# Kernel tuning notes

Measured on AMD Instinct MI355X. Metric: run time of the kernel, lower is better.

## Reference

```python
import jax, jax.numpy as jnp
import numpy as np

FLOAT_MAX = 3.4e38
FLOAT_MIN = -3.4e38


def _net1_forward(link_mtx, action_mask, col_table, rel_table, graph_weight,
                  graph_bias, Wk, Wq, Wv, fc_w, table_ids, l_col_ids, r_col_ids):
    emb = rel_table.shape[1]

    # ---- graph_forward: GCN layer over relation graph, mean pooling ----
    # link_mtx: [B, R, R], rel_table: [R, E]
    support = jnp.einsum('bnm,me->bne', link_mtx, rel_table)          # [B, R, E]
    out_graph = jax.nn.relu(support @ graph_weight + graph_bias)      # [B, R, G]
    pooled = out_graph.mean(axis=1)                                   # [B, G]

    # ---- tree_forward: batched left-deep join trees via scan over depth ----
    # table_ids: [B, T, D+1]; col ids: [B, T, D, C]
    r_tabs = rel_table[table_ids[..., 1:]]                            # [B, T, D, E]
    l_cols = col_table[l_col_ids].mean(axis=-2)                       # [B, T, D, E] (mean pooling of joined cols)
    r_cols = col_table[r_col_ids].mean(axis=-2)                       # [B, T, D, E]
    xs = (jnp.moveaxis(r_tabs, 2, 0), jnp.moveaxis(l_cols, 2, 0),
          jnp.moveaxis(r_cols, 2, 0))                                  # each [D, B, T, E]
    init = rel_table[table_ids[..., 0]]                               # [B, T, E] leftmost leaf

    def step(prev, x):
        rte, lce, rce = x
        # query_emb = cat([l_table, l_col, r_col, r_table]) -> 4 tokens
        q = jnp.stack([prev, lce, rce, rte], axis=-2)                 # [B, T, 4, E]
        K = q @ Wk
        Q = q @ Wq
        V = q @ Wv
        scores = jnp.einsum('btqe,btke->btqk', Q, K) / emb            # note: /emb, not /sqrt(emb)
        attn = jax.nn.softmax(scores, axis=-1)
        out = jnp.einsum('btqk,btke->btqe', attn, V).sum(axis=-2)     # sum over query rows -> [B, T, E]
        return out, None

    final, _ = jax.lax.scan(step, init, xs)                           # [B, T, E]
    tree_emb = final.sum(axis=1)                                      # sum over subtrees -> [B, E]

    logits = jnp.concatenate([pooled, tree_emb], axis=1) @ fc_w       # [B, A]
    inf_mask = jnp.clip(jnp.log(action_mask), FLOAT_MIN, FLOAT_MAX)
    return inf_mask + logits


def setup_inputs() -> dict:
    key = jax.random.key(0)
    ks = jax.random.split(key, 12)
    B, T, D, C = 8, 8, 16, 2
    num_rel, num_col, num_actions = 4096, 20000, 4096
    emb, gdim = 64, 64
    std = 0.05
    return {
        'link_mtx': jax.random.uniform(ks[0], (B, num_rel, num_rel), dtype=jnp.float32),
        'action_mask': jnp.ones((B, num_actions), dtype=jnp.float32),
        'col_table': jax.random.normal(ks[1], (num_col, emb), dtype=jnp.float32) * std,
        'rel_table': jax.random.normal(ks[2], (num_rel, emb), dtype=jnp.float32) * std,
        'graph_weight': jax.random.normal(ks[3], (emb, gdim), dtype=jnp.float32) * std,
        'graph_bias': jnp.zeros((gdim,), dtype=jnp.float32),
        'Wk': jax.random.normal(ks[4], (emb, emb), dtype=jnp.float32) * std,
        'Wq': jax.random.normal(ks[5], (emb, emb), dtype=jnp.float32) * std,
        'Wv': jax.random.normal(ks[6], (emb, emb), dtype=jnp.float32) * std,
        'fc_w': jax.random.normal(ks[7], (gdim + emb, num_actions), dtype=jnp.float32) * std,
        'table_ids': jax.random.randint(ks[8], (B, T, D + 1), 0, num_rel),
        'l_col_ids': jax.random.randint(ks[9], (B, T, D, C), 0, num_col),
        'r_col_ids': jax.random.randint(ks[10], (B, T, D, C), 0, num_col),
    }


def reference(link_mtx, action_mask, col_table, rel_table, graph_weight,
              graph_bias, Wk, Wq, Wv, fc_w, table_ids, l_col_ids, r_col_ids):
    return _net1_forward(link_mtx, action_mask, col_table, rel_table, graph_weight,
                         graph_bias, Wk, Wq, Wv, fc_w, table_ids, l_col_ids, r_col_ids)
```

## Files before the change

### kernel.cpp

```cpp
#include <hip/hip_runtime.h>
#include <hip/hip_bf16.h>
#include <stdint.h>

typedef __attribute__((ext_vector_type(8))) short short8;
typedef __attribute__((ext_vector_type(4))) float f32x4;

union FragU { short8 s; __hip_bfloat162 h[4]; };
union BU { uint4 u; short8 s; };

__device__ __forceinline__ unsigned short f2bf(float f) {
  union { float f; unsigned int u; } v; v.f = f;
  unsigned int r = v.u + 0x7fffu + ((v.u >> 16) & 1u);
  return (unsigned short)(r >> 16);
}
__device__ __forceinline__ float bf2f(unsigned short h) {
  union { unsigned int u; float f; } v; v.u = ((unsigned int)h) << 16;
  return v.f;
}

#define GLOAD_LDS16(gp, lp) \
  __builtin_amdgcn_global_load_lds((const __attribute__((address_space(1))) void*)(gp), \
                                   (__attribute__((address_space(3))) void*)(lp), 16, 0, 0)

__global__ void k_prep(const float* __restrict__ rel, const float* __restrict__ GW,
                       unsigned short* __restrict__ bTf, float* __restrict__ accums) {
  __shared__ float tile[64][65];
  __shared__ float gws[64][64];
  __shared__ float relgw[64][64];
  const int j = blockIdx.x;
  const int t = threadIdx.x;
#pragma unroll
  for (int p = 0; p < 16; ++p) {
    int elem = p * 256 + t;
    int kk = elem >> 6, ee = elem & 63;
    tile[kk][ee] = rel[(j * 64 + kk) * 64 + ee];
    ((float*)gws)[elem] = GW[elem];
  }
  __syncthreads();
  {
    const int e = t >> 2, chunk = t & 3;
    for (int i = 0; i < 16; ++i) {
      float acc = 0.f;
#pragma unroll
      for (int ii = 0; ii < 64; ++ii) acc += tile[chunk * 16 + i][ii] * gws[ii][e];
      relgw[chunk * 16 + i][e] = acc;
    }
  }
  __syncthreads();
#pragma unroll
  for (int m = 0; m < 2; ++m) {
    const int f = t * 2 + m;
    const int nt = f >> 7, kc = (f >> 6) & 1, ln = f & 63;
    const int g = ln >> 4, r = ln & 15;
    union { unsigned short u16[8]; uint4 v; } pk;
#pragma unroll
    for (int s = 0; s < 8; ++s) pk.u16[s] = f2bf(relgw[kc * 32 + g * 8 + s][nt * 16 + r]);
    *(uint4*)(bTf + (size_t)j * 4096 + f * 8) = pk.v;
  }
  if (j == 0) {
    accums[t] = 0.f; accums[t + 256] = 0.f; accums[t + 512] = 0.f; accums[t + 768] = 0.f;
  }
}

__global__ __launch_bounds__(256, 2) void k_main(
    const float* __restrict__ link, const unsigned short* __restrict__ bTf,
    const float* __restrict__ gbias, float* __restrict__ pooled_sum,
    const float* __restrict__ col_table, const float* __restrict__ rel_table,
    const float* __restrict__ Wk, const float* __restrict__ Wq, const float* __restrict__ Wv,
    const int* __restrict__ table_ids, const int* __restrict__ l_ids,
    const int* __restrict__ r_ids, float* __restrict__ tree_emb) {
  __shared__ union {
    struct { char a[4][2][8192]; } g;
    struct { unsigned short W3b[3 * 4096]; float qT[4][64][4]; } tr;
  } sm;

  const int t = threadIdx.x;
  const int lane = t & 63;
  const int wid = t >> 6;

  if (blockIdx.x >= 16) {
    const int gid = blockIdx.x - 16;
    const int b = gid >> 6;
    const int rb = gid & 63;
    const int rowG0 = rb * 64 + wid * 16;
    const int phase = (gid * 4 + wid + b * 9) & 31;
    const int g = lane >> 4;
    const int r = lane & 15;
    const uint32_t fr = (uint32_t)((r & 7) << 4);

    const char* linkb = (const char*)(link + ((size_t)b << 24));
    const char* bTfb = (const char*)bTf;
    const int a_r2 = lane >> 5;
    const uint32_t a_wb = (uint32_t)((lane & 31) * 16);

    char* a0buf = sm.g.a[wid][0];
    char* a1buf = sm.g.a[wid][1];

    f32x4 acc[4];
#pragma unroll
    for (int nt = 0; nt < 4; ++nt) acc[nt] = (f32x4){0.f, 0.f, 0.f, 0.f};
    uint4 bq[16];

#define STAGEA(ab_, tta) do {                                              \
    const size_t ka = (size_t)(tta) * 512;          \
    _Pragma("unroll")                                                      \
    for (int j = 0; j < 8; ++j) {                                          \
      const int wlrow = 2 * j + a_r2;                                      \
      const uint32_t cb = a_wb ^ ((uint32_t)(wlrow & 7) << 4);             \
      GLOAD_LDS16(linkb + (size_t)(rowG0 + wlrow) * 16384 + ka + cb,       \
                  (ab_) + j * 1024);                                       \
    }                                                                      \
  } while (0)

#define LOADB(tta) do {                                                    \
    const char* bb = bTfb + (size_t)(tta) * 16384 + lane * 16;             \
    _Pragma("unroll")                                                      \
    for (int j = 0; j < 8; ++j) {                                          \
      bq[j]     = *(const uint4*)(bb + j * 1024);                          \
      bq[8 + j] = *(const uint4*)(bb + 8192 + j * 1024);                   \
    }                                                                      \
  } while (0)

#define COMPUTEW(ab_) do {                                                 \
    const char* ar = (ab_) + r * 512;                                      \
    _Pragma("unroll")                                                      \
    for (int kh = 0; kh < 2; ++kh) {                                       \
      _Pragma("unroll")                                                    \
      for (int kc = 0; kc < 2; ++kc) {                                     \
        const uint32_t o0 = ((uint32_t)(kh * 256 + kc * 128 + g * 32)) ^ fr; \
        const f32x4 a0 = *(const f32x4*)(ar + o0);                         \
        const f32x4 a1 = *(const f32x4*)(ar + (o0 ^ 16));                  \
        FragU f;                                                           \
        f.h[0] = __float22bfloat162_rn(float2{a0[0], a0[1]});              \
        f.h[1] = __float22bfloat162_rn(float2{a0[2], a0[3]});              \
        f.h[2] = __float22bfloat162_rn(float2{a1[0], a1[1]});              \
        f.h[3] = __float22bfloat162_rn(float2{a1[2], a1[3]});              \
        _Pragma("unroll")                                                  \
        for (int nt = 0; nt < 4; ++nt) {                                   \
          BU bu; bu.u = bq[kh * 8 + nt * 2 + kc];                          \
          acc[nt] = __builtin_amdgcn_mfma_f32_16x16x32_bf16(f.s, bu.s, acc[nt], 0, 0, 0); \
        }                                                                  \
      }                                                                    \
    }                                                                      \
  } while (0)

    STAGEA(a0buf, phase);
    for (int it2 = 0; it2 < 16; ++it2) {
      const int te = 2 * it2;
      LOADB((te + phase) & 31);
      STAGEA(a1buf, (te + 1 + phase) & 31);
      asm volatile("s_waitcnt vmcnt(8)" ::: "memory");
      COMPUTEW(a0buf);
      LOADB((te + 1 + phase) & 31);
      if (it2 < 15) {
        STAGEA(a0buf, (te + 2 + phase) & 31);
        asm volatile("s_waitcnt vmcnt(8)" ::: "memory");
      } else {
        asm volatile("s_waitcnt vmcnt(0)" ::: "memory");
      }
      COMPUTEW(a1buf);
    }

#pragma unroll
    for (int nt = 0; nt < 4; ++nt) {
      const float gbv = gbias[nt * 16 + r];
      float s = 0.f;
#pragma unroll
      for (int j = 0; j < 4; ++j) s += fmaxf(acc[nt][j] + gbv, 0.f);
      s += __shfl_xor(s, 16);
      s += __shfl_xor(s, 32);
      if (g == 0) atomicAdd(&pooled_sum[b * 64 + nt * 16 + r], s);
    }
  } else {
    const int e = lane;
    for (int i = t; i < 3 * 4096; i += 256) {
      float v;
      if (i < 4096) v = Wk[i];
      else if (i < 8192) v = Wq[i - 4096];
      else v = Wv[i - 8192];
      sm.tr.W3b[i] = f2bf(v);
    }
    __syncthreads();

    const int tree = blockIdx.x * 4 + wid;
    const int b = tree >> 3;
    const int* tid = table_ids + tree * 17;
    const int* lid = l_ids + tree * 32;
    const int* rid = r_ids + tree * 32;

    float prev = rel_table[tid[0] * 64 + e];

    for (int d = 0; d < 16; ++d) {
      const int l0 = lid[d * 2], l1 = lid[d * 2 + 1];
      const int r0 = rid[d * 2], r1 = rid[d * 2 + 1];
      const float lce = 0.5f * (col_table[l0 * 64 + e] + col_table[l1 * 64 + e]);
      const float rce = 0.5f * (col_table[r0 * 64 + e] + col_table[r1 * 64 + e]);
      const float rte = rel_table[tid[1 + d] * 64 + e];
      float4 qv0; qv0.x = prev; qv0.y = lce; qv0.z = rce; qv0.w = rte;
      *(float4*)&sm.tr.qT[wid][e][0] = qv0;
      __syncthreads();

      float K[4] = {0, 0, 0, 0}, Q[4] = {0, 0, 0, 0}, V[4] = {0, 0, 0, 0};
#pragma unroll 8
      for (int i = 0; i < 64; ++i) {
        const f32x4 qv = *(const f32x4*)&sm.tr.qT[wid][i][0];
        const float wk = bf2f(sm.tr.W3b[i * 64 + e]);
        const float wq = bf2f(sm.tr.W3b[4096 + i * 64 + e]);
        const float wvv = bf2f(sm.tr.W3b[8192 + i * 64 + e]);
#pragma unroll
        for (int j = 0; j < 4; ++j) {
          K[j] += qv[j] * wk;
          Q[j] += qv[j] * wq;
          V[j] += qv[j] * wvv;
        }
      }

      float sc[4][4];
#pragma unroll
      for (int j = 0; j < 4; ++j)
#pragma unroll
        for (int k = 0; k < 4; ++k) {
          float p = Q[j] * K[k];
          p += __shfl_xor(p, 1);  p += __shfl_xor(p, 2);  p += __shfl_xor(p, 4);
          p += __shfl_xor(p, 8);  p += __shfl_xor(p, 16); p += __shfl_xor(p, 32);
          sc[j][k] = p * (1.f / 64.f);
        }

      float wsum[4] = {0, 0, 0, 0};
#pragma unroll
      for (int j = 0; j < 4; ++j) {
        float mx = fmaxf(fmaxf(sc[j][0], sc[j][1]), fmaxf(sc[j][2], sc[j][3]));
        float a0 = __expf(sc[j][0] - mx), a1 = __expf(sc[j][1] - mx);
        float a2 = __expf(sc[j][2] - mx), a3 = __expf(sc[j][3] - mx);
        float inv = 1.f / (a0 + a1 + a2 + a3);
        wsum[0] += a0 * inv; wsum[1] += a1 * inv; wsum[2] += a2 * inv; wsum[3] += a3 * inv;
      }

      prev = wsum[0] * V[0] + wsum[1] * V[1] + wsum[2] * V[2] + wsum[3] * V[3];
      __syncthreads();
    }
    atomicAdd(&tree_emb[b * 64 + e], prev);
  }
}

__global__ void k_final(const float* __restrict__ action_mask, const float* __restrict__ fc_w,
                        const float* __restrict__ pooled_sum, const float* __restrict__ tree_emb,
                        float* __restrict__ out) {
  __shared__ float c[128];
  const int b = blockIdx.x >> 4;
  const int a = ((blockIdx.x & 15) << 8) + threadIdx.x;
  if (threadIdx.x < 128) {
    c[threadIdx.x] = (threadIdx.x < 64) ? pooled_sum[b * 64 + threadIdx.x] * (1.f / 4096.f)
                                        : tree_emb[b * 64 + threadIdx.x - 64];
  }
  __syncthreads();
  float acc = 0.f;
  for (int i = 0; i < 128; ++i) acc += c[i] * fc_w[i * 4096 + a];
  const float m = action_mask[b * 4096 + a];
  float lg = __logf(m);
  lg = fminf(fmaxf(lg, -3.4e38f), 3.4e38f);
  out[b * 4096 + a] = lg + acc;
}

extern "C" void kernel_launch(void* const* d_in, const int* in_sizes, int n_in,
                              void* d_out, int out_size, void* d_ws, size_t ws_size,
                              hipStream_t stream) {
  const float* link = (const float*)d_in[0];
  const float* mask = (const float*)d_in[1];
  const float* col = (const float*)d_in[2];
  const float* rel = (const float*)d_in[3];
  const float* GW = (const float*)d_in[4];
  const float* gb = (const float*)d_in[5];
  const float* Wk = (const float*)d_in[6];
  const float* Wq = (const float*)d_in[7];
  const float* Wv = (const float*)d_in[8];
  const float* fcw = (const float*)d_in[9];
  const int* tids = (const int*)d_in[10];
  const int* lids = (const int*)d_in[11];
  const int* rids = (const int*)d_in[12];
  float* out = (float*)d_out;

  unsigned short* bTf = (unsigned short*)d_ws;
  float* accums = (float*)((char*)d_ws + 512 * 1024);
  float* pooled_sum = accums;
  float* tree = accums + 512;

  hipLaunchKernelGGL(k_prep, dim3(64), dim3(256), 0, stream, rel, GW, bTf, accums);
  hipLaunchKernelGGL(k_main, dim3(528), dim3(256), 0, stream,
                     link, bTf, gb, pooled_sum,
                     col, rel, Wk, Wq, Wv, tids, lids, rids, tree);
  hipLaunchKernelGGL(k_final, dim3(128), dim3(256), 0, stream, mask, fcw, pooled_sum, tree, out);
}
```

Measured before the change: 142.9 us.

## Move tree attention blocks into prep kernel and zero accumulators via memset

The 16 tree-scan blocks move out of the main GEMM kernel and into the prep kernel, which now runs 80 blocks: 64 for the rel·GW precompute and 16 for the tree recurrence. Accumulator zeroing becomes a hipMemsetAsync instead of being done by block 0 of prep. The aim is to keep the slow serial tree blocks off the main kernel's critical path and to shrink its shared-memory union to the A staging buffers only. The cost is an extra memset launch, and the tree work now serialises with prep before the main kernel starts.

```diff
diff --git a/kernel.cpp b/kernel.cpp
--- a/kernel.cpp
+++ b/kernel.cpp
@@ -23,83 +23,152 @@
                                    (__attribute__((address_space(3))) void*)(lp), 16, 0, 0)
 
 __global__ void k_prep(const float* __restrict__ rel, const float* __restrict__ GW,
-                       unsigned short* __restrict__ bTf, float* __restrict__ accums) {
-  __shared__ float tile[64][65];
-  __shared__ float gws[64][64];
-  __shared__ float relgw[64][64];
-  const int j = blockIdx.x;
-  const int t = threadIdx.x;
-#pragma unroll
-  for (int p = 0; p < 16; ++p) {
-    int elem = p * 256 + t;
-    int kk = elem >> 6, ee = elem & 63;
-    tile[kk][ee] = rel[(j * 64 + kk) * 64 + ee];
-    ((float*)gws)[elem] = GW[elem];
-  }
-  __syncthreads();
-  {
-    const int e = t >> 2, chunk = t & 3;
-    for (int i = 0; i < 16; ++i) {
-      float acc = 0.f;
-#pragma unroll
-      for (int ii = 0; ii < 64; ++ii) acc += tile[chunk * 16 + i][ii] * gws[ii][e];
-      relgw[chunk * 16 + i][e] = acc;
-    }
-  }
-  __syncthreads();
-#pragma unroll
-  for (int m = 0; m < 2; ++m) {
-    const int f = t * 2 + m;
-    const int nt = f >> 7, kc = (f >> 6) & 1, ln = f & 63;
-    const int g = ln >> 4, r = ln & 15;
-    union { unsigned short u16[8]; uint4 v; } pk;
-#pragma unroll
-    for (int s = 0; s < 8; ++s) pk.u16[s] = f2bf(relgw[kc * 32 + g * 8 + s][nt * 16 + r]);
-    *(uint4*)(bTf + (size_t)j * 4096 + f * 8) = pk.v;
-  }
-  if (j == 0) {
-    accums[t] = 0.f; accums[t + 256] = 0.f; accums[t + 512] = 0.f; accums[t + 768] = 0.f;
-  }
-}
-
-__global__ __launch_bounds__(256, 2) void k_main(
-    const float* __restrict__ link, const unsigned short* __restrict__ bTf,
-    const float* __restrict__ gbias, float* __restrict__ pooled_sum,
-    const float* __restrict__ col_table, const float* __restrict__ rel_table,
-    const float* __restrict__ Wk, const float* __restrict__ Wq, const float* __restrict__ Wv,
-    const int* __restrict__ table_ids, const int* __restrict__ l_ids,
-    const int* __restrict__ r_ids, float* __restrict__ tree_emb) {
+                       unsigned short* __restrict__ bTf,
+                       const float* __restrict__ col_table, const float* __restrict__ rel_table,
+                       const float* __restrict__ Wk, const float* __restrict__ Wq,
+                       const float* __restrict__ Wv,
+                       const int* __restrict__ table_ids, const int* __restrict__ l_ids,
+                       const int* __restrict__ r_ids, float* __restrict__ tree_emb) {
   __shared__ union {
-    struct { char a[4][2][8192]; } g;
+    struct { float tile[64][65]; float gws[64][64]; float relgw[64][64]; } p;
     struct { unsigned short W3b[3 * 4096]; float qT[4][64][4]; } tr;
   } sm;
-
   const int t = threadIdx.x;
   const int lane = t & 63;
   const int wid = t >> 6;
 
-  if (blockIdx.x >= 16) {
-    const int gid = blockIdx.x - 16;
-    const int b = gid >> 6;
-    const int rb = gid & 63;
-    const int rowG0 = rb * 64 + wid * 16;
-    const int phase = (gid * 4 + wid + b * 9) & 31;
-    const int g = lane >> 4;
-    const int r = lane & 15;
-    const uint32_t fr = (uint32_t)((r & 7) << 4);
-
-    const char* linkb = (const char*)(link + ((size_t)b << 24));
-    const char* bTfb = (const char*)bTf;
-    const int a_r2 = lane >> 5;
-    const uint32_t a_wb = (uint32_t)((lane & 31) * 16);
-
-    char* a0buf = sm.g.a[wid][0];
-    char* a1buf = sm.g.a[wid][1];
-
-    f32x4 acc[4];
-#pragma unroll
-    for (int nt = 0; nt < 4; ++nt) acc[nt] = (f32x4){0.f, 0.f, 0.f, 0.f};
-    uint4 bq[16];
+  if (blockIdx.x < 64) {
+    const int j = blockIdx.x;
+#pragma unroll
+    for (int p = 0; p < 16; ++p) {
+      int elem = p * 256 + t;
+      int kk = elem >> 6, ee = elem & 63;
+      sm.p.tile[kk][ee] = rel[(j * 64 + kk) * 64 + ee];
+      ((float*)sm.p.gws)[elem] = GW[elem];
+    }
+    __syncthreads();
+    {
+      const int e = t >> 2, chunk = t & 3;
+      for (int i = 0; i < 16; ++i) {
+        float acc = 0.f;
+#pragma unroll
+        for (int ii = 0; ii < 64; ++ii) acc += sm.p.tile[chunk * 16 + i][ii] * sm.p.gws[ii][e];
+        sm.p.relgw[chunk * 16 + i][e] = acc;
+      }
+    }
+    __syncthreads();
+#pragma unroll
+    for (int m = 0; m < 2; ++m) {
+      const int f = t * 2 + m;
+      const int nt = f >> 7, kc = (f >> 6) & 1, ln = f & 63;
+      const int g = ln >> 4, r = ln & 15;
+      union { unsigned short u16[8]; uint4 v; } pk;
+#pragma unroll
+      for (int s = 0; s < 8; ++s) pk.u16[s] = f2bf(sm.p.relgw[kc * 32 + g * 8 + s][nt * 16 + r]);
+      *(uint4*)(bTf + (size_t)j * 4096 + f * 8) = pk.v;
+    }
+  } else {
+    const int e = lane;
+    for (int i = t; i < 3 * 4096; i += 256) {
+      float v;
+      if (i < 4096) v = Wk[i];
+      else if (i < 8192) v = Wq[i - 4096];
+      else v = Wv[i - 8192];
+      sm.tr.W3b[i] = f2bf(v);
+    }
+    __syncthreads();
+
+    const int tree = (blockIdx.x - 64) * 4 + wid;
+    const int b = tree >> 3;
+    const int* tid = table_ids + tree * 17;
+    const int* lid = l_ids + tree * 32;
+    const int* rid = r_ids + tree * 32;
+
+    float prev = rel_table[tid[0] * 64 + e];
+
+    for (int d = 0; d < 16; ++d) {
+      const int l0 = lid[d * 2], l1 = lid[d * 2 + 1];
+      const int r0 = rid[d * 2], r1 = rid[d * 2 + 1];
+      const float lce = 0.5f * (col_table[l0 * 64 + e] + col_table[l1 * 64 + e]);
+      const float rce = 0.5f * (col_table[r0 * 64 + e] + col_table[r1 * 64 + e]);
+      const float rte = rel_table[tid[1 + d] * 64 + e];
+      float4 qv0; qv0.x = prev; qv0.y = lce; qv0.z = rce; qv0.w = rte;
+      *(float4*)&sm.tr.qT[wid][e][0] = qv0;
+      __syncthreads();
+
+      float K[4] = {0, 0, 0, 0}, Q[4] = {0, 0, 0, 0}, V[4] = {0, 0, 0, 0};
+#pragma unroll 8
+      for (int i = 0; i < 64; ++i) {
+        const f32x4 qv = *(const f32x4*)&sm.tr.qT[wid][i][0];
+        const float wk = bf2f(sm.tr.W3b[i * 64 + e]);
+        const float wq = bf2f(sm.tr.W3b[4096 + i * 64 + e]);
+        const float wvv = bf2f(sm.tr.W3b[8192 + i * 64 + e]);
+#pragma unroll
+        for (int j = 0; j < 4; ++j) {
+          K[j] += qv[j] * wk;
+          Q[j] += qv[j] * wq;
+          V[j] += qv[j] * wvv;
+        }
+      }
+
+      float sc[4][4];
+#pragma unroll
+      for (int j = 0; j < 4; ++j)
+#pragma unroll
+        for (int k = 0; k < 4; ++k) {
+          float p = Q[j] * K[k];
+          p += __shfl_xor(p, 1);  p += __shfl_xor(p, 2);  p += __shfl_xor(p, 4);
+          p += __shfl_xor(p, 8);  p += __shfl_xor(p, 16); p += __shfl_xor(p, 32);
+          sc[j][k] = p * (1.f / 64.f);
+        }
+
+      float wsum[4] = {0, 0, 0, 0};
+#pragma unroll
+      for (int j = 0; j < 4; ++j) {
+        float mx = fmaxf(fmaxf(sc[j][0], sc[j][1]), fmaxf(sc[j][2], sc[j][3]));
+        float a0 = __expf(sc[j][0] - mx), a1 = __expf(sc[j][1] - mx);
+        float a2 = __expf(sc[j][2] - mx), a3 = __expf(sc[j][3] - mx);
+        float inv = 1.f / (a0 + a1 + a2 + a3);
+        wsum[0] += a0 * inv; wsum[1] += a1 * inv; wsum[2] += a2 * inv; wsum[3] += a3 * inv;
+      }
+
+      prev = wsum[0] * V[0] + wsum[1] * V[1] + wsum[2] * V[2] + wsum[3] * V[3];
+      __syncthreads();
+    }
+    atomicAdd(&tree_emb[b * 64 + e], prev);
+  }
+}
+
+__global__ __launch_bounds__(256, 2) void k_main(
+    const float* __restrict__ link, const unsigned short* __restrict__ bTf,
+    const float* __restrict__ gbias, float* __restrict__ pooled_sum) {
+  __shared__ char aLds[4][2][8192];
+
+  const int t = threadIdx.x;
+  const int lane = t & 63;
+  const int wid = t >> 6;
+
+  const int gid = blockIdx.x;
+  const int b = gid >> 6;
+  const int rb = gid & 63;
+  const int rowG0 = rb * 64 + wid * 16;
+  const int phase = (gid * 4 + wid + b * 9) & 31;
+  const int g = lane >> 4;
+  const int r = lane & 15;
+  const uint32_t fr = (uint32_t)((r & 7) << 4);
+
+  const char* linkb = (const char*)(link + ((size_t)b << 24));
+  const char* bTfb = (const char*)bTf;
+  const int a_r2 = lane >> 5;
+  const uint32_t a_wb = (uint32_t)((lane & 31) * 16);
+
+  char* a0buf = aLds[wid][0];
+  char* a1buf = aLds[wid][1];
+
+  f32x4 acc[4];
+#pragma unroll
+  for (int nt = 0; nt < 4; ++nt) acc[nt] = (f32x4){0.f, 0.f, 0.f, 0.f};
+  uint4 bq[16];
 
 #define STAGEA(ab_, tta) do {                                              \
     const size_t ka = (size_t)(tta) * 512;          \
@@ -144,102 +213,32 @@
     }                                                                      \
   } while (0)
 
-    STAGEA(a0buf, phase);
-    for (int it2 = 0; it2 < 16; ++it2) {
-      const int te = 2 * it2;
-      LOADB((te + phase) & 31);
-      STAGEA(a1buf, (te + 1 + phase) & 31);
+  STAGEA(a0buf, phase);
+  for (int it2 = 0; it2 < 16; ++it2) {
+    const int te = 2 * it2;
+    LOADB((te + phase) & 31);
+    STAGEA(a1buf, (te + 1 + phase) & 31);
+    asm volatile("s_waitcnt vmcnt(8)" ::: "memory");
+    COMPUTEW(a0buf);
+    LOADB((te + 1 + phase) & 31);
+    if (it2 < 15) {
+      STAGEA(a0buf, (te + 2 + phase) & 31);
       asm volatile("s_waitcnt vmcnt(8)" ::: "memory");
-      COMPUTEW(a0buf);
-      LOADB((te + 1 + phase) & 31);
-      if (it2 < 15) {
-        STAGEA(a0buf, (te + 2 + phase) & 31);
-        asm volatile("s_waitcnt vmcnt(8)" ::: "memory");
-      } else {
-        asm volatile("s_waitcnt vmcnt(0)" ::: "memory");
-      }
-      COMPUTEW(a1buf);
-    }
-
-#pragma unroll
-    for (int nt = 0; nt < 4; ++nt) {
-      const float gbv = gbias[nt * 16 + r];
-      float s = 0.f;
-#pragma unroll
-      for (int j = 0; j < 4; ++j) s += fmaxf(acc[nt][j] + gbv, 0.f);
-      s += __shfl_xor(s, 16);
-      s += __shfl_xor(s, 32);
-      if (g == 0) atomicAdd(&pooled_sum[b * 64 + nt * 16 + r], s);
-    }
-  } else {
-    const int e = lane;
-    for (int i = t; i < 3 * 4096; i += 256) {
-      float v;
-      if (i < 4096) v = Wk[i];
-      else if (i < 8192) v = Wq[i - 4096];
-      else v = Wv[i - 8192];
-      sm.tr.W3b[i] = f2bf(v);
-    }
-    __syncthreads();
-
-    const int tree = blockIdx.x * 4 + wid;
-    const int b = tree >> 3;
-    const int* tid = table_ids + tree * 17;
-    const int* lid = l_ids + tree * 32;
-    const int* rid = r_ids + tree * 32;
-
-    float prev = rel_table[tid[0] * 64 + e];
-
-    for (int d = 0; d < 16; ++d) {
-      const int l0 = lid[d * 2], l1 = lid[d * 2 + 1];
-      const int r0 = rid[d * 2], r1 = rid[d * 2 + 1];
-      const float lce = 0.5f * (col_table[l0 * 64 + e] + col_table[l1 * 64 + e]);
-      const float rce = 0.5f * (col_table[r0 * 64 + e] + col_table[r1 * 64 + e]);
-      const float rte = rel_table[tid[1 + d] * 64 + e];
-      float4 qv0; qv0.x = prev; qv0.y = lce; qv0.z = rce; qv0.w = rte;
-      *(float4*)&sm.tr.qT[wid][e][0] = qv0;
-      __syncthreads();
-
-      float K[4] = {0, 0, 0, 0}, Q[4] = {0, 0, 0, 0}, V[4] = {0, 0, 0, 0};
-#pragma unroll 8
-      for (int i = 0; i < 64; ++i) {
-        const f32x4 qv = *(const f32x4*)&sm.tr.qT[wid][i][0];
-        const float wk = bf2f(sm.tr.W3b[i * 64 + e]);
-        const float wq = bf2f(sm.tr.W3b[4096 + i * 64 + e]);
-        const float wvv = bf2f(sm.tr.W3b[8192 + i * 64 + e]);
-#pragma unroll
-        for (int j = 0; j < 4; ++j) {
-          K[j] += qv[j] * wk;
-          Q[j] += qv[j] * wq;
-          V[j] += qv[j] * wvv;
-        }
-      }
-
-      float sc[4][4];
-#pragma unroll
-      for (int j = 0; j < 4; ++j)
-#pragma unroll
-        for (int k = 0; k < 4; ++k) {
-          float p = Q[j] * K[k];
-          p += __shfl_xor(p, 1);  p += __shfl_xor(p, 2);  p += __shfl_xor(p, 4);
-          p += __shfl_xor(p, 8);  p += __shfl_xor(p, 16); p += __shfl_xor(p, 32);
-          sc[j][k] = p * (1.f / 64.f);
-        }
-
-      float wsum[4] = {0, 0, 0, 0};
-#pragma unroll
-      for (int j = 0; j < 4; ++j) {
-        float mx = fmaxf(fmaxf(sc[j][0], sc[j][1]), fmaxf(sc[j][2], sc[j][3]));
-        float a0 = __expf(sc[j][0] - mx), a1 = __expf(sc[j][1] - mx);
-        float a2 = __expf(sc[j][2] - mx), a3 = __expf(sc[j][3] - mx);
-        float inv = 1.f / (a0 + a1 + a2 + a3);
-        wsum[0] += a0 * inv; wsum[1] += a1 * inv; wsum[2] += a2 * inv; wsum[3] += a3 * inv;
-      }
-
-      prev = wsum[0] * V[0] + wsum[1] * V[1] + wsum[2] * V[2] + wsum[3] * V[3];
-      __syncthreads();
-    }
-    atomicAdd(&tree_emb[b * 64 + e], prev);
+    } else {
+      asm volatile("s_waitcnt vmcnt(0)" ::: "memory");
+    }
+    COMPUTEW(a1buf);
+  }
+
+#pragma unroll
+  for (int nt = 0; nt < 4; ++nt) {
+    const float gbv = gbias[nt * 16 + r];
+    float s = 0.f;
+#pragma unroll
+    for (int j = 0; j < 4; ++j) s += fmaxf(acc[nt][j] + gbv, 0.f);
+    s += __shfl_xor(s, 16);
+    s += __shfl_xor(s, 32);
+    if (g == 0) atomicAdd(&pooled_sum[b * 64 + nt * 16 + r], s);
   }
 }
 
@@ -285,9 +284,10 @@
   float* pooled_sum = accums;
   float* tree = accums + 512;
 
-  hipLaunchKernelGGL(k_prep, dim3(64), dim3(256), 0, stream, rel, GW, bTf, accums);
-  hipLaunchKernelGGL(k_main, dim3(528), dim3(256), 0, stream,
-                     link, bTf, gb, pooled_sum,
-                     col, rel, Wk, Wq, Wv, tids, lids, rids, tree);
+  hipMemsetAsync(accums, 0, 1024 * sizeof(float), stream);
+  hipLaunchKernelGGL(k_prep, dim3(80), dim3(256), 0, stream,
+                     rel, GW, bTf, col, rel, Wk, Wq, Wv, tids, lids, rids, tree);
+  hipLaunchKernelGGL(k_main, dim3(512), dim3(256), 0, stream,
+                     link, bTf, gb, pooled_sum);
   hipLaunchKernelGGL(k_final, dim3(128), dim3(256), 0, stream, mask, fcw, pooled_sum, tree, out);
 }
```

Result: slower. 209.5 us (+46.6%).
